# Optimization experiments

Measured on AMD Instinct MI355X. Metric: run time of the kernel, lower is better.

Reference implementation:

```python
import jax, jax.numpy as jnp
import numpy as np

D = 768          # model dim (ViT-Base)
H = 12           # num heads
DH = 64          # head dim
DFF = 4 * D      # mlp hidden
SMAX = 1024      # max sequence length in the packed batch
LENS = np.array([1024, 896, 768, 640, 512, 448, 256, 64], dtype=np.int32)
TOTAL = int(LENS.sum())  # 4608
LN_EPS = 1e-6
NEG = -1e30


def _ln(x, w, b):
    mu = jnp.mean(x, axis=-1, keepdims=True)
    var = jnp.mean(jnp.square(x - mu), axis=-1, keepdims=True)
    return (x - mu) * jax.lax.rsqrt(var + LN_EPS) * w + b


def setup_inputs() -> dict:
    key = jax.random.key(0)
    ks = jax.random.split(key, 16)
    s = 0.02
    cu = jnp.asarray(np.concatenate([[0], np.cumsum(LENS)]).astype(np.int32))
    return {
        "x": jax.random.normal(ks[0], (TOTAL, D), jnp.float32),
        "norm1_w": jnp.ones((D,), jnp.float32),
        "norm1_b": jnp.zeros((D,), jnp.float32),
        "qkv_w": jax.random.normal(ks[1], (3 * D, D), jnp.float32) * s,
        "qkv_b": jnp.zeros((3 * D,), jnp.float32),
        "proj_w": jax.random.normal(ks[2], (D, D), jnp.float32) * s,
        "proj_b": jnp.zeros((D,), jnp.float32),
        "ls1_gamma": jax.random.normal(ks[3], (D,), jnp.float32) * 0.1,
        "norm2_w": jnp.ones((D,), jnp.float32),
        "norm2_b": jnp.zeros((D,), jnp.float32),
        "fc1_w": jax.random.normal(ks[4], (DFF, D), jnp.float32) * s,
        "fc1_b": jnp.zeros((DFF,), jnp.float32),
        "fc2_w": jax.random.normal(ks[5], (D, DFF), jnp.float32) * s,
        "fc2_b": jnp.zeros((D,), jnp.float32),
        "ls2_gamma": jax.random.normal(ks[6], (D,), jnp.float32) * 0.1,
        "cu_seqlens": cu,
    }


def reference(x, norm1_w, norm1_b, qkv_w, qkv_b, proj_w, proj_b, ls1_gamma,
              norm2_w, norm2_b, fc1_w, fc1_b, fc2_w, fc2_b, ls2_gamma,
              cu_seqlens):
    total = x.shape[0]
    B = cu_seqlens.shape[0] - 1
    tok = jnp.arange(total)
    seg = jnp.searchsorted(cu_seqlens[1:], tok, side="right")  # [Total]
    pos = tok - cu_seqlens[seg]                                 # [Total]
    lens = cu_seqlens[1:] - cu_seqlens[:-1]                     # [B]

    # --- attention branch ---
    xn = _ln(x, norm1_w, norm1_b)
    qkv = (xn @ qkv_w.T + qkv_b).reshape(total, 3, H, DH)
    q, k, v = qkv[:, 0], qkv[:, 1], qkv[:, 2]                   # [Total,H,DH]

    # pad packed ragged tokens to [B, SMAX, H, DH]
    def pad(t):
        return jnp.zeros((B, SMAX, H, DH), t.dtype).at[seg, pos].set(t)
    qp, kp, vp = pad(q), pad(k), pad(v)

    valid = jnp.arange(SMAX)[None, :] < lens[:, None]           # [B,SMAX]
    scores = jnp.einsum("bqhd,bkhd->bhqk", qp, kp) * (DH ** -0.5)
    scores = jnp.where(valid[:, None, None, :], scores, NEG)
    attn = jax.nn.softmax(scores, axis=-1)
    out = jnp.einsum("bhqk,bkhd->bqhd", attn, vp)
    out = out[seg, pos].reshape(total, D)                       # back to packed

    attn_out = out @ proj_w.T + proj_b
    x = x + ls1_gamma * attn_out

    # --- mlp branch ---
    xn2 = _ln(x, norm2_w, norm2_b)
    h = jax.nn.gelu(xn2 @ fc1_w.T + fc1_b, approximate=False)
    h = h @ fc2_w.T + fc2_b
    return x + ls2_gamma * h
```

## Files before the change

### kernel.cpp

```cpp
#include <hip/hip_runtime.h>
#include <hip/hip_bf16.h>
#include <stdint.h>

#define D 768
#define HEADS 12
#define DHEAD 64
#define DFF 3072
#define TOTAL 4608
#define NSEG 8

typedef __bf16 bf16;
typedef __bf16 bf16x8 __attribute__((ext_vector_type(8)));
typedef __bf16 bf16x4 __attribute__((ext_vector_type(4)));
typedef float f32x4 __attribute__((ext_vector_type(4)));

__device__ __forceinline__ void gld_lds16(const void* g, void* l) {
  __builtin_amdgcn_global_load_lds(
      (const __attribute__((address_space(1))) void*)g,
      (__attribute__((address_space(3))) void*)(uintptr_t)l, 16, 0, 0);
}

__global__ __launch_bounds__(256) void cvt_all_kernel(
    const float* __restrict__ a, const float* __restrict__ b,
    const float* __restrict__ c, const float* __restrict__ d,
    bf16* __restrict__ out, int nA, int nAB, int nABC, int nTot) {
  int i = blockIdx.x * blockDim.x + threadIdx.x;
  if (i >= nTot) return;
  const float* src;
  int j;
  if (i < nA) { src = a; j = i; }
  else if (i < nAB) { src = b; j = i - nA; }
  else if (i < nABC) { src = c; j = i - nAB; }
  else { src = d; j = i - nABC; }
  float4 v = ((const float4*)src)[j];
  bf16x4 o;
  o[0] = (bf16)v.x; o[1] = (bf16)v.y; o[2] = (bf16)v.z; o[3] = (bf16)v.w;
  ((bf16x4*)out)[i] = o;
}

__global__ __launch_bounds__(256) void ln_kernel(
    const float* __restrict__ x, const float* __restrict__ w,
    const float* __restrict__ b, bf16* __restrict__ out) {
  __shared__ float red[8];
  int row = blockIdx.x;
  const float* xr = x + (size_t)row * D;
  int t = threadIdx.x;
  float v[3];
  float s = 0.f, s2 = 0.f;
#pragma unroll
  for (int j = 0; j < 3; j++) {
    v[j] = xr[t + 256 * j];
    s += v[j]; s2 += v[j] * v[j];
  }
#pragma unroll
  for (int m = 1; m <= 32; m <<= 1) {
    s += __shfl_xor(s, m);
    s2 += __shfl_xor(s2, m);
  }
  int wave = t >> 6, lane = t & 63;
  if (lane == 0) { red[wave] = s; red[4 + wave] = s2; }
  __syncthreads();
  s = red[0] + red[1] + red[2] + red[3];
  s2 = red[4] + red[5] + red[6] + red[7];
  float mu = s * (1.f / 768.f);
  float var = s2 * (1.f / 768.f) - mu * mu;
  float rstd = rsqrtf(var + 1e-6f);
#pragma unroll
  for (int j = 0; j < 3; j++) {
    int c = t + 256 * j;
    out[(size_t)row * D + c] = (bf16)((v[j] - mu) * rstd * w[c] + b[c]);
  }
}

__device__ __forceinline__ float fast_gelu(float v) {
  float u = v * (0.7978845608f + 0.0356774081f * v * v);
  float e = exp2f(2.8853900818f * u);
  float th = 1.f - 2.f * __builtin_amdgcn_rcpf(1.f + e);
  return 0.5f * v * (1.f + th);
}

template <int MODE, int TN, int BK, int GX, int GY>
__global__ __launch_bounds__(256) void gemm_kernel(
    const bf16* __restrict__ A, const bf16* __restrict__ W,
    const float* __restrict__ bias, const float* __restrict__ res,
    const float* __restrict__ gamma, bf16* __restrict__ outb,
    float* __restrict__ outf, int N, int K) {
  constexpr int NJ = TN / 32;
  constexpr int KH = BK / 32;
  constexpr int CG = BK / 8;
  constexpr int SH = (BK == 32) ? 1 : 0;
  constexpr int LPR = BK / 8;
  constexpr int RS = 64 / LPR;
  constexpr int RB = TN / 4;
  __shared__ __align__(16) bf16 As[2][128 * BK];
  __shared__ __align__(16) bf16 Bs[2][TN * BK];

  const int g = blockIdx.x;
  const int xc = g & 7, q = g >> 3;
  const int bx = q % GX, by = xc + 8 * (q / GX);
  if (by >= GY) return;
  const int m0 = by * 128, n0 = bx * TN;

  const int t = threadIdx.x, wave = t >> 6, lane = t & 63;
  const int quad = lane >> 4, l16 = lane & 15;
  const int wm = (wave & 1) * 64, wn = (wave >> 1) * (TN / 2);

  const int ar = lane / LPR, ac = lane % LPR;
  const int acg = ac ^ (((wave * 32 + ar) >> SH) & (CG - 1));
  const int bcg = ac ^ (((wave * RB + ar) >> SH) & (CG - 1));
  const bf16* gA = A + (size_t)(m0 + wave * 32 + ar) * K + acg * 8;
  const bf16* gB = W + (size_t)(n0 + wave * RB + ar) * K + bcg * 8;

  auto stage = [&](int buf) {
#pragma unroll
    for (int n = 0; n < 32 / RS; n++)
      gld_lds16(gA + (size_t)n * RS * K, &As[buf][(wave * 32 + n * RS) * BK]);
#pragma unroll
    for (int n = 0; n < RB / RS; n++)
      gld_lds16(gB + (size_t)n * RS * K, &Bs[buf][(wave * RB + n * RS) * BK]);
    gA += BK; gB += BK;
  };

  stage(0);

  f32x4 acc[4][NJ] = {};
  int cur = 0;
  for (int k0 = 0; k0 < K; k0 += BK) {
    __syncthreads();
    if (k0 + BK < K) stage(cur ^ 1);
    const bf16* as = As[cur];
    const bf16* bs = Bs[cur];
    bf16x8 af[KH][4], bg[KH][NJ];
#pragma unroll
    for (int kh = 0; kh < KH; kh++) {
#pragma unroll
      for (int i = 0; i < 4; i++) {
        int R = wm + i * 16 + l16;
        af[kh][i] = *(const bf16x8*)&as[R * BK + 8 * ((kh * 4 + quad) ^ ((R >> SH) & (CG - 1)))];
      }
#pragma unroll
      for (int j = 0; j < NJ; j++) {
        int R = wn + j * 16 + l16;
        bg[kh][j] = *(const bf16x8*)&bs[R * BK + 8 * ((kh * 4 + quad) ^ ((R >> SH) & (CG - 1)))];
      }
    }
#pragma unroll
    for (int kh = 0; kh < KH; kh++)
#pragma unroll
      for (int i = 0; i < 4; i++)
#pragma unroll
        for (int j = 0; j < NJ; j++)
          acc[i][j] = __builtin_amdgcn_mfma_f32_16x16x32_bf16(af[kh][i], bg[kh][j], acc[i][j], 0, 0, 0);
    cur ^= 1;
  }

#pragma unroll
  for (int i = 0; i < 4; i++)
#pragma unroll
    for (int j = 0; j < NJ; j++)
#pragma unroll
      for (int r = 0; r < 4; r++) {
        int row = m0 + wm + i * 16 + quad * 4 + r;
        int col = n0 + wn + j * 16 + l16;
        float v = acc[i][j][r] + bias[col];
        if (MODE == 0) {
          outb[(size_t)row * N + col] = (bf16)v;
        } else if (MODE == 1) {
          outf[(size_t)row * N + col] = res[(size_t)row * N + col] + gamma[col] * v;
        } else {
          outb[(size_t)row * N + col] = (bf16)fast_gelu(v);
        }
      }
}

__global__ __launch_bounds__(256) void attn_kernel(
    const bf16* __restrict__ qkv, const int* __restrict__ cu,
    bf16* __restrict__ attn) {
  __shared__ __align__(16) bf16 Ks[64][72];
  __shared__ __align__(16) bf16 VTs[64][64];

  const int qt = blockIdx.x, h = blockIdx.y;
  const int tok0 = qt * 64;
  int b = 0;
  while (cu[b + 1] <= tok0) b++;
  const int s0 = cu[b], S = cu[b + 1] - s0;

  const int t = threadIdx.x, wave = t >> 6, lane = t & 63;
  const int quad = lane >> 4, l16 = lane & 15;

  const size_t qrow = (size_t)(tok0 + wave * 16 + l16) * (3 * D) + h * 64;
  const bf16x8 bq0 = *(const bf16x8*)&qkv[qrow + quad * 8];
  const bf16x8 bq1 = *(const bf16x8*)&qkv[qrow + 32 + quad * 8];

  const int srow = t >> 2, sc0 = (t & 3) * 16;
  const size_t kbase = (size_t)(s0 + srow) * (3 * D) + h * 64 + sc0 + D;
  const int vr0 = (t & 15) * 4, vd0 = (t >> 4) * 4;
  const size_t vbase = (size_t)(s0 + vr0) * (3 * D) + h * 64 + vd0 + 2 * D;
  const int kB0 = ((vr0 >> 5) << 5) | (((vr0 >> 2) & 3) << 3) | (((vr0 >> 4) & 1) << 2);

  bf16x8 kr0 = *(const bf16x8*)&qkv[kbase];
  bf16x8 kr1 = *(const bf16x8*)&qkv[kbase + 8];
  bf16x4 vp[4];
#pragma unroll
  for (int i = 0; i < 4; i++)
    vp[i] = *(const bf16x4*)&qkv[vbase + (size_t)i * (3 * D)];

  f32x4 Oacc[4] = {};
  float li = 0.f;
  const float SC = 0.125f * 1.44269504089f;

  for (int kb = 0; kb < S; kb += 64) {
    __syncthreads();
    *(bf16x8*)&Ks[srow][sc0] = kr0;
    *(bf16x8*)&Ks[srow][sc0 + 8] = kr1;
#pragma unroll
    for (int j = 0; j < 4; j++) {
      int d = vd0 + j;
      bf16x4 w;
      w[0] = vp[0][j]; w[1] = vp[1][j]; w[2] = vp[2][j]; w[3] = vp[3][j];
      *(bf16x4*)&VTs[d][kB0 ^ ((d & 7) * 8)] = w;
    }
    __syncthreads();

    if (kb + 64 < S) {
      const size_t koff = kbase + (size_t)(kb + 64) * (3 * D);
      const size_t voff = vbase + (size_t)(kb + 64) * (3 * D);
      kr0 = *(const bf16x8*)&qkv[koff];
      kr1 = *(const bf16x8*)&qkv[koff + 8];
#pragma unroll
      for (int i = 0; i < 4; i++)
        vp[i] = *(const bf16x4*)&qkv[voff + (size_t)i * (3 * D)];
    }

    f32x4 sac[4];
#pragma unroll
    for (int nt = 0; nt < 4; nt++) {
      bf16x8 ak0 = *(const bf16x8*)&Ks[nt * 16 + l16][quad * 8];
      bf16x8 ak1 = *(const bf16x8*)&Ks[nt * 16 + l16][32 + quad * 8];
      f32x4 z = {};
      z = __builtin_amdgcn_mfma_f32_16x16x32_bf16(ak0, bq0, z, 0, 0, 0);
      sac[nt] = __builtin_amdgcn_mfma_f32_16x16x32_bf16(ak1, bq1, z, 0, 0, 0);
    }

    bf16x8 bv0, bv1;
    float ls = 0.f;
#pragma unroll
    for (int r = 0; r < 4; r++) {
      float e0 = exp2f(sac[0][r] * SC);
      float e1 = exp2f(sac[1][r] * SC);
      float e2 = exp2f(sac[2][r] * SC);
      float e3 = exp2f(sac[3][r] * SC);
      ls += (e0 + e1) + (e2 + e3);
      bv0[r] = (bf16)e0; bv0[4 + r] = (bf16)e1;
      bv1[r] = (bf16)e2; bv1[4 + r] = (bf16)e3;
    }
    li += ls;

    const int vsw = (l16 & 7) * 8;
#pragma unroll
    for (int dt = 0; dt < 4; dt++) {
      bf16x8 av0 = *(const bf16x8*)&VTs[dt * 16 + l16][(quad * 8) ^ vsw];
      bf16x8 av1 = *(const bf16x8*)&VTs[dt * 16 + l16][(32 + quad * 8) ^ vsw];
      Oacc[dt] = __builtin_amdgcn_mfma_f32_16x16x32_bf16(av0, bv0, Oacc[dt], 0, 0, 0);
      Oacc[dt] = __builtin_amdgcn_mfma_f32_16x16x32_bf16(av1, bv1, Oacc[dt], 0, 0, 0);
    }
  }

  li += __shfl_xor(li, 16);
  li += __shfl_xor(li, 32);
  const float inv = 1.f / li;

  __syncthreads();
  bf16(*Osh)[72] = (bf16(*)[72])Ks;
  const int orow = wave * 16 + l16;
#pragma unroll
  for (int dt = 0; dt < 4; dt++) {
    int dg = dt * 16 + quad * 4;
    bf16x4 w;
#pragma unroll
    for (int r = 0; r < 4; r++) w[r] = (bf16)(Oacc[dt][r] * inv);
    *(bf16x4*)&Osh[orow][dg ^ ((l16 & 7) * 8)] = w;
  }
  const int osw = (l16 & 7) * 8;
  bf16x8 o0 = *(const bf16x8*)&Osh[orow][(quad * 16) ^ osw];
  bf16x8 o1 = *(const bf16x8*)&Osh[orow][(quad * 16 + 8) ^ osw];
  const size_t obase = (size_t)(tok0 + orow) * D + h * 64 + quad * 16;
  *(bf16x8*)&attn[obase] = o0;
  *(bf16x8*)&attn[obase + 8] = o1;
}

extern "C" void kernel_launch(void* const* d_in, const int* in_sizes, int n_in,
                              void* d_out, int out_size, void* d_ws,
                              size_t ws_size, hipStream_t stream) {
  const float* x       = (const float*)d_in[0];
  const float* norm1_w = (const float*)d_in[1];
  const float* norm1_b = (const float*)d_in[2];
  const float* qkv_w   = (const float*)d_in[3];
  const float* qkv_b   = (const float*)d_in[4];
  const float* proj_w  = (const float*)d_in[5];
  const float* proj_b  = (const float*)d_in[6];
  const float* ls1     = (const float*)d_in[7];
  const float* norm2_w = (const float*)d_in[8];
  const float* norm2_b = (const float*)d_in[9];
  const float* fc1_w   = (const float*)d_in[10];
  const float* fc1_b   = (const float*)d_in[11];
  const float* fc2_w   = (const float*)d_in[12];
  const float* fc2_b   = (const float*)d_in[13];
  const float* ls2     = (const float*)d_in[14];
  const int*   cu      = (const int*)d_in[15];
  float* out = (float*)d_out;

  char* ws = (char*)d_ws;
  size_t off = 0;
  auto alloc = [&](size_t bytes) {
    void* p = ws + off;
    off += (bytes + 255) & ~(size_t)255;
    return p;
  };
  bf16* w_qkv  = (bf16*)alloc((size_t)3 * D * D * 2);
  bf16* w_proj = (bf16*)alloc((size_t)D * D * 2);
  bf16* w_fc1  = (bf16*)alloc((size_t)DFF * D * 2);
  bf16* w_fc2  = (bf16*)alloc((size_t)D * DFF * 2);
  bf16* xn     = (bf16*)alloc((size_t)TOTAL * D * 2);
  bf16* qkv    = (bf16*)alloc((size_t)TOTAL * 3 * D * 2);
  bf16* attnb  = (bf16*)alloc((size_t)TOTAL * D * 2);
  float* x1    = (float*)alloc((size_t)TOTAL * D * 4);
  bf16* hbuf   = qkv;

  {
    int nA   = 3 * D * D / 4;
    int nAB  = nA + D * D / 4;
    int nABC = nAB + DFF * D / 4;
    int nTot = nABC + D * DFF / 4;
    cvt_all_kernel<<<(nTot + 255) / 256, 256, 0, stream>>>(
        qkv_w, proj_w, fc1_w, fc2_w, w_qkv, nA, nAB, nABC, nTot);
  }

  ln_kernel<<<TOTAL, 256, 0, stream>>>(x, norm1_w, norm1_b, xn);

  constexpr int GY = TOTAL / 128;
  constexpr int GYP = ((GY + 7) / 8) * 8;

  gemm_kernel<0, 128, 64, 18, GY><<<18 * GYP, 256, 0, stream>>>(
      xn, w_qkv, qkv_b, nullptr, nullptr, qkv, nullptr, 3 * D, D);

  dim3 ga(TOTAL / 64, HEADS);
  attn_kernel<<<ga, 256, 0, stream>>>(qkv, cu, attnb);

  gemm_kernel<1, 64, 64, 12, GY><<<12 * GYP, 256, 0, stream>>>(
      attnb, w_proj, proj_b, x, ls1, nullptr, x1, D, D);

  ln_kernel<<<TOTAL, 256, 0, stream>>>(x1, norm2_w, norm2_b, xn);

  gemm_kernel<2, 128, 64, 24, GY><<<24 * GYP, 256, 0, stream>>>(
      xn, w_fc1, fc1_b, nullptr, nullptr, hbuf, nullptr, DFF, D);

  gemm_kernel<1, 64, 64, 12, GY><<<12 * GYP, 256, 0, stream>>>(
      hbuf, w_fc2, fc2_b, x1, ls2, nullptr, out, D, DFF);
}
```

Baseline: 262.1 us.

## Split attention key loop across two wave groups per block and merge partials

The attention block grows from 256 to 512 threads. The two groups of four waves each take alternate 64-key tiles, using double-sized shared K/V buffers. At the end the second group writes its partial O accumulators and row sums to shared memory, and the first group adds them and writes the output. This halves the serial key-loop length per block, which suits long sequences. The cost is larger blocks, more shared memory, an extra reduction through shared memory, and possibly lower occupancy.

```diff
diff --git a/kernel.cpp b/kernel.cpp
--- a/kernel.cpp
+++ b/kernel.cpp
@@ -173,11 +173,11 @@
       }
 }
 
-__global__ __launch_bounds__(256) void attn_kernel(
+__global__ __launch_bounds__(512) void attn_kernel(
     const bf16* __restrict__ qkv, const int* __restrict__ cu,
     bf16* __restrict__ attn) {
-  __shared__ __align__(16) bf16 Ks[64][72];
-  __shared__ __align__(16) bf16 VTs[64][64];
+  __shared__ __align__(16) bf16 Ks[2][64][72];
+  __shared__ __align__(16) bf16 VTs[2][64][64];
 
   const int qt = blockIdx.x, h = blockIdx.y;
   const int tok0 = qt * 64;
@@ -185,46 +185,62 @@
   while (cu[b + 1] <= tok0) b++;
   const int s0 = cu[b], S = cu[b + 1] - s0;
 
-  const int t = threadIdx.x, wave = t >> 6, lane = t & 63;
+  const int t = threadIdx.x;
+  const int grp = t >> 8;
+  const int tl = t & 255;
+  const int wave = tl >> 6, lane = t & 63;
   const int quad = lane >> 4, l16 = lane & 15;
 
   const size_t qrow = (size_t)(tok0 + wave * 16 + l16) * (3 * D) + h * 64;
   const bf16x8 bq0 = *(const bf16x8*)&qkv[qrow + quad * 8];
   const bf16x8 bq1 = *(const bf16x8*)&qkv[qrow + 32 + quad * 8];
 
-  const int srow = t >> 2, sc0 = (t & 3) * 16;
+  const int srow = tl >> 2, sc0 = (tl & 3) * 16;
   const size_t kbase = (size_t)(s0 + srow) * (3 * D) + h * 64 + sc0 + D;
-  const int vr0 = (t & 15) * 4, vd0 = (t >> 4) * 4;
+  const int vr0 = (tl & 15) * 4, vd0 = (tl >> 4) * 4;
   const size_t vbase = (size_t)(s0 + vr0) * (3 * D) + h * 64 + vd0 + 2 * D;
   const int kB0 = ((vr0 >> 5) << 5) | (((vr0 >> 2) & 3) << 3) | (((vr0 >> 4) & 1) << 2);
 
-  bf16x8 kr0 = *(const bf16x8*)&qkv[kbase];
-  bf16x8 kr1 = *(const bf16x8*)&qkv[kbase + 8];
-  bf16x4 vp[4];
-#pragma unroll
-  for (int i = 0; i < 4; i++)
-    vp[i] = *(const bf16x4*)&qkv[vbase + (size_t)i * (3 * D)];
+  const int ntile = S >> 6;
+  const int nit = (ntile + 1) >> 1;
+
+  bf16x8 kr0 = {}, kr1 = {};
+  bf16x4 vp[4] = {};
+  if (grp * 64 < S) {
+    const size_t k0 = kbase + (size_t)(grp * 64) * (3 * D);
+    kr0 = *(const bf16x8*)&qkv[k0];
+    kr1 = *(const bf16x8*)&qkv[k0 + 8];
+    const size_t v0 = vbase + (size_t)(grp * 64) * (3 * D);
+#pragma unroll
+    for (int i = 0; i < 4; i++)
+      vp[i] = *(const bf16x4*)&qkv[v0 + (size_t)i * (3 * D)];
+  }
 
   f32x4 Oacc[4] = {};
   float li = 0.f;
   const float SC = 0.125f * 1.44269504089f;
 
-  for (int kb = 0; kb < S; kb += 64) {
+  int kb = grp * 64;
+  for (int it = 0; it < nit; it++, kb += 128) {
+    const bool act = kb < S;
     __syncthreads();
-    *(bf16x8*)&Ks[srow][sc0] = kr0;
-    *(bf16x8*)&Ks[srow][sc0 + 8] = kr1;
-#pragma unroll
-    for (int j = 0; j < 4; j++) {
-      int d = vd0 + j;
-      bf16x4 w;
-      w[0] = vp[0][j]; w[1] = vp[1][j]; w[2] = vp[2][j]; w[3] = vp[3][j];
-      *(bf16x4*)&VTs[d][kB0 ^ ((d & 7) * 8)] = w;
+    if (act) {
+      *(bf16x8*)&Ks[grp][srow][sc0] = kr0;
+      *(bf16x8*)&Ks[grp][srow][sc0 + 8] = kr1;
+#pragma unroll
+      for (int j = 0; j < 4; j++) {
+        int d = vd0 + j;
+        bf16x4 w;
+        w[0] = vp[0][j]; w[1] = vp[1][j]; w[2] = vp[2][j]; w[3] = vp[3][j];
+        *(bf16x4*)&VTs[grp][d][kB0 ^ ((d & 7) * 8)] = w;
+      }
     }
     __syncthreads();
-
-    if (kb + 64 < S) {
-      const size_t koff = kbase + (size_t)(kb + 64) * (3 * D);
-      const size_t voff = vbase + (size_t)(kb + 64) * (3 * D);
+    if (!act) continue;
+
+    if (kb + 128 < S) {
+      const size_t koff = kbase + (size_t)(kb + 128) * (3 * D);
+      const size_t voff = vbase + (size_t)(kb + 128) * (3 * D);
       kr0 = *(const bf16x8*)&qkv[koff];
       kr1 = *(const bf16x8*)&qkv[koff + 8];
 #pragma unroll
@@ -235,8 +251,8 @@
     f32x4 sac[4];
 #pragma unroll
     for (int nt = 0; nt < 4; nt++) {
-      bf16x8 ak0 = *(const bf16x8*)&Ks[nt * 16 + l16][quad * 8];
-      bf16x8 ak1 = *(const bf16x8*)&Ks[nt * 16 + l16][32 + quad * 8];
+      bf16x8 ak0 = *(const bf16x8*)&Ks[grp][nt * 16 + l16][quad * 8];
+      bf16x8 ak1 = *(const bf16x8*)&Ks[grp][nt * 16 + l16][32 + quad * 8];
       f32x4 z = {};
       z = __builtin_amdgcn_mfma_f32_16x16x32_bf16(ak0, bq0, z, 0, 0, 0);
       sac[nt] = __builtin_amdgcn_mfma_f32_16x16x32_bf16(ak1, bq1, z, 0, 0, 0);
@@ -259,18 +275,33 @@
     const int vsw = (l16 & 7) * 8;
 #pragma unroll
     for (int dt = 0; dt < 4; dt++) {
-      bf16x8 av0 = *(const bf16x8*)&VTs[dt * 16 + l16][(quad * 8) ^ vsw];
-      bf16x8 av1 = *(const bf16x8*)&VTs[dt * 16 + l16][(32 + quad * 8) ^ vsw];
+      bf16x8 av0 = *(const bf16x8*)&VTs[grp][dt * 16 + l16][(quad * 8) ^ vsw];
+      bf16x8 av1 = *(const bf16x8*)&VTs[grp][dt * 16 + l16][(32 + quad * 8) ^ vsw];
       Oacc[dt] = __builtin_amdgcn_mfma_f32_16x16x32_bf16(av0, bv0, Oacc[dt], 0, 0, 0);
       Oacc[dt] = __builtin_amdgcn_mfma_f32_16x16x32_bf16(av1, bv1, Oacc[dt], 0, 0, 0);
     }
   }
+
+  __syncthreads();
+  float* osum = (float*)VTs;
+  float* lsum = (float*)&Ks[1][0][0];
+  if (grp) {
+#pragma unroll
+    for (int dt = 0; dt < 4; dt++)
+      *(f32x4*)&osum[tl * 16 + dt * 4] = Oacc[dt];
+    lsum[tl] = li;
+  }
+  __syncthreads();
+  if (grp) return;
+#pragma unroll
+  for (int dt = 0; dt < 4; dt++)
+    Oacc[dt] += *(const f32x4*)&osum[tl * 16 + dt * 4];
+  li += lsum[tl];
 
   li += __shfl_xor(li, 16);
   li += __shfl_xor(li, 32);
   const float inv = 1.f / li;
 
-  __syncthreads();
   bf16(*Osh)[72] = (bf16(*)[72])Ks;
   const int orow = wave * 16 + l16;
 #pragma unroll
@@ -345,7 +376,7 @@
       xn, w_qkv, qkv_b, nullptr, nullptr, qkv, nullptr, 3 * D, D);
 
   dim3 ga(TOTAL / 64, HEADS);
-  attn_kernel<<<ga, 256, 0, stream>>>(qkv, cu, attnb);
+  attn_kernel<<<ga, 512, 0, stream>>>(qkv, cu, attnb);
 
   gemm_kernel<1, 64, 64, 12, GY><<<12 * GYP, 256, 0, stream>>>(
       attnb, w_proj, proj_b, x, ls1, nullptr, x1, D, D);
```

Result: slower. 270.6 us (+3.3%).

## Double-buffer K/V shared-memory tiles in attention kernel

Applied to the files above, without the earlier changes.

Gives the K and V^T LDS tiles two buffers so each loop iteration needs one barrier instead of two. All LDS fragments for the current tile are read into registers first, then the next tile is staged into the other buffer and the tile after that is prefetched from global, overlapping the staging with MFMA and exp work. This raises LDS use and register pressure, which may lower occupancy. The epilogue still reuses Ks as the output staging area.

```diff
diff --git a/kernel.cpp b/kernel.cpp
--- a/kernel.cpp
+++ b/kernel.cpp
@@ -176,8 +176,8 @@
 __global__ __launch_bounds__(256) void attn_kernel(
     const bf16* __restrict__ qkv, const int* __restrict__ cu,
     bf16* __restrict__ attn) {
-  __shared__ __align__(16) bf16 Ks[64][72];
-  __shared__ __align__(16) bf16 VTs[64][64];
+  __shared__ __align__(16) bf16 Ks[2][64][72];
+  __shared__ __align__(16) bf16 VTs[2][64][64];
 
   const int qt = blockIdx.x, h = blockIdx.y;
   const int tok0 = qt * 64;
@@ -198,6 +198,8 @@
   const size_t vbase = (size_t)(s0 + vr0) * (3 * D) + h * 64 + vd0 + 2 * D;
   const int kB0 = ((vr0 >> 5) << 5) | (((vr0 >> 2) & 3) << 3) | (((vr0 >> 4) & 1) << 2);
 
+  const int ntile = S >> 6;
+
   bf16x8 kr0 = *(const bf16x8*)&qkv[kbase];
   bf16x8 kr1 = *(const bf16x8*)&qkv[kbase + 8];
   bf16x4 vp[4];
@@ -205,41 +207,62 @@
   for (int i = 0; i < 4; i++)
     vp[i] = *(const bf16x4*)&qkv[vbase + (size_t)i * (3 * D)];
 
-  f32x4 Oacc[4] = {};
-  float li = 0.f;
-  const float SC = 0.125f * 1.44269504089f;
-
-  for (int kb = 0; kb < S; kb += 64) {
-    __syncthreads();
-    *(bf16x8*)&Ks[srow][sc0] = kr0;
-    *(bf16x8*)&Ks[srow][sc0 + 8] = kr1;
+  auto stageKV = [&](int buf) {
+    *(bf16x8*)&Ks[buf][srow][sc0] = kr0;
+    *(bf16x8*)&Ks[buf][srow][sc0 + 8] = kr1;
 #pragma unroll
     for (int j = 0; j < 4; j++) {
       int d = vd0 + j;
       bf16x4 w;
       w[0] = vp[0][j]; w[1] = vp[1][j]; w[2] = vp[2][j]; w[3] = vp[3][j];
-      *(bf16x4*)&VTs[d][kB0 ^ ((d & 7) * 8)] = w;
-    }
+      *(bf16x4*)&VTs[buf][d][kB0 ^ ((d & 7) * 8)] = w;
+    }
+  };
+  auto loadKV = [&](int tile) {
+    const size_t koff = kbase + (size_t)tile * 64 * (3 * D);
+    const size_t voff = vbase + (size_t)tile * 64 * (3 * D);
+    kr0 = *(const bf16x8*)&qkv[koff];
+    kr1 = *(const bf16x8*)&qkv[koff + 8];
+#pragma unroll
+    for (int i = 0; i < 4; i++)
+      vp[i] = *(const bf16x4*)&qkv[voff + (size_t)i * (3 * D)];
+  };
+
+  stageKV(0);
+  if (ntile > 1) loadKV(1);
+
+  f32x4 Oacc[4] = {};
+  float li = 0.f;
+  const float SC = 0.125f * 1.44269504089f;
+  const int vsw = (l16 & 7) * 8;
+
+  for (int it = 0; it < ntile; it++) {
+    const int cur = it & 1;
     __syncthreads();
 
-    if (kb + 64 < S) {
-      const size_t koff = kbase + (size_t)(kb + 64) * (3 * D);
-      const size_t voff = vbase + (size_t)(kb + 64) * (3 * D);
-      kr0 = *(const bf16x8*)&qkv[koff];
-      kr1 = *(const bf16x8*)&qkv[koff + 8];
-#pragma unroll
-      for (int i = 0; i < 4; i++)
-        vp[i] = *(const bf16x4*)&qkv[voff + (size_t)i * (3 * D)];
+    bf16x8 ak0[4], ak1[4], av0[4], av1[4];
+#pragma unroll
+    for (int nt = 0; nt < 4; nt++) {
+      ak0[nt] = *(const bf16x8*)&Ks[cur][nt * 16 + l16][quad * 8];
+      ak1[nt] = *(const bf16x8*)&Ks[cur][nt * 16 + l16][32 + quad * 8];
+    }
+#pragma unroll
+    for (int dt = 0; dt < 4; dt++) {
+      av0[dt] = *(const bf16x8*)&VTs[cur][dt * 16 + l16][(quad * 8) ^ vsw];
+      av1[dt] = *(const bf16x8*)&VTs[cur][dt * 16 + l16][(32 + quad * 8) ^ vsw];
+    }
+
+    if (it + 1 < ntile) {
+      stageKV(cur ^ 1);
+      if (it + 2 < ntile) loadKV(it + 2);
     }
 
     f32x4 sac[4];
 #pragma unroll
     for (int nt = 0; nt < 4; nt++) {
-      bf16x8 ak0 = *(const bf16x8*)&Ks[nt * 16 + l16][quad * 8];
-      bf16x8 ak1 = *(const bf16x8*)&Ks[nt * 16 + l16][32 + quad * 8];
       f32x4 z = {};
-      z = __builtin_amdgcn_mfma_f32_16x16x32_bf16(ak0, bq0, z, 0, 0, 0);
-      sac[nt] = __builtin_amdgcn_mfma_f32_16x16x32_bf16(ak1, bq1, z, 0, 0, 0);
+      z = __builtin_amdgcn_mfma_f32_16x16x32_bf16(ak0[nt], bq0, z, 0, 0, 0);
+      sac[nt] = __builtin_amdgcn_mfma_f32_16x16x32_bf16(ak1[nt], bq1, z, 0, 0, 0);
     }
 
     bf16x8 bv0, bv1;
@@ -256,13 +279,10 @@
     }
     li += ls;
 
-    const int vsw = (l16 & 7) * 8;
 #pragma unroll
     for (int dt = 0; dt < 4; dt++) {
-      bf16x8 av0 = *(const bf16x8*)&VTs[dt * 16 + l16][(quad * 8) ^ vsw];
-      bf16x8 av1 = *(const bf16x8*)&VTs[dt * 16 + l16][(32 + quad * 8) ^ vsw];
-      Oacc[dt] = __builtin_amdgcn_mfma_f32_16x16x32_bf16(av0, bv0, Oacc[dt], 0, 0, 0);
-      Oacc[dt] = __builtin_amdgcn_mfma_f32_16x16x32_bf16(av1, bv1, Oacc[dt], 0, 0, 0);
+      Oacc[dt] = __builtin_amdgcn_mfma_f32_16x16x32_bf16(av0[dt], bv0, Oacc[dt], 0, 0, 0);
+      Oacc[dt] = __builtin_amdgcn_mfma_f32_16x16x32_bf16(av1[dt], bv1, Oacc[dt], 0, 0, 0);
     }
   }
 
```

After: 263.8 us. Within noise of the previous version (+0.7%).
